# Performance work log

Measured on AMD Instinct MI355X. Metric: run time of the kernel, lower is better.

The kernel has to match this reference:

```python
import jax, jax.numpy as jnp
import numpy as np

D_MODEL = 1024
NUM_HEADS = 16
D_K = D_MODEL // NUM_HEADS
NEG_INF = -1e9


def setup_inputs() -> dict:
    key = jax.random.key(0)
    ks = jax.random.split(key, 9)
    B, S, D = 4, 2048, D_MODEL
    scale = 1.0 / np.sqrt(D)
    inp = {
        "x": jax.random.normal(ks[0], (B, S, D), dtype=jnp.float32),
        "Wq": jax.random.normal(ks[1], (D, D), dtype=jnp.float32) * scale,
        "bq": jnp.zeros((D,), dtype=jnp.float32),
        "Wk": jax.random.normal(ks[2], (D, D), dtype=jnp.float32) * scale,
        "bk": jnp.zeros((D,), dtype=jnp.float32),
        "Wv": jax.random.normal(ks[3], (D, D), dtype=jnp.float32) * scale,
        "bv": jnp.zeros((D,), dtype=jnp.float32),
        "Wo": jax.random.normal(ks[4], (D, D), dtype=jnp.float32) * scale,
        "bo": jnp.zeros((D,), dtype=jnp.float32),
    }
    return inp


def reference(x, Wq, bq, Wk, bk, Wv, bv, Wo, bo):
    B, S, D = x.shape
    H, dk = NUM_HEADS, D_K
    # padding mask: token is pad if any feature == 0; shape [B,1,1,S] (keys)
    mask = (x == 0).any(axis=-1)[:, None, None, :]

    def split_heads(t):  # [B,S,D] -> [B,H,S,dk]
        return t.reshape(B, S, H, dk).transpose(0, 2, 1, 3)

    q = split_heads(x @ Wq + bq)
    k = split_heads(x @ Wk + bk)
    v = split_heads(x @ Wv + bv)

    scores = jnp.einsum("bhqd,bhkd->bhqk", q, k) / np.sqrt(dk).astype(x.dtype)
    scores = jnp.where(mask, jnp.asarray(NEG_INF, x.dtype), scores)
    weights = jax.nn.softmax(scores, axis=-1)
    context = jnp.einsum("bhqk,bhkd->bhqd", weights, v)
    context = context.transpose(0, 2, 1, 3).reshape(B, S, D)
    return context @ Wo + bo
```

## Files before the change

kernel.cpp:

```cpp
#include <hip/hip_runtime.h>
#include <cstdint>
#include <cstddef>

static constexpr int Bz = 4, S = 2048, Dm = 1024, H = 16, DK = 64;
static constexpr int M = Bz * S;

typedef __attribute__((ext_vector_type(8))) short bf16x8;
typedef __attribute__((ext_vector_type(4))) float f32x4;

__device__ __forceinline__ unsigned short f2b(float f) {
    unsigned u = __float_as_uint(f);
    return (unsigned short)((u + 0x7FFFu + ((u >> 16) & 1u)) >> 16);
}

__device__ __forceinline__ unsigned cvtpk(float lo, float hi) {
    unsigned r;
    asm("v_cvt_pk_bf16_f32 %0, %1, %2" : "=v"(r) : "v"(lo), "v"(hi));
    return r;
}

__device__ __forceinline__ float fexp2(float x) {
#if __has_builtin(__builtin_amdgcn_exp2f)
    return __builtin_amdgcn_exp2f(x);
#else
    float r;
    asm("v_exp_f32 %0, %1" : "=v"(r) : "v"(x));
    return r;
#endif
}

__device__ __forceinline__ void gld_lds16(const void* g, void* l) {
    __builtin_amdgcn_global_load_lds(
        (const __attribute__((address_space(1))) unsigned int*)g,
        (__attribute__((address_space(3))) unsigned int*)l, 16, 0, 0);
}

__global__ __launch_bounds__(256) void k_convx(const float* __restrict__ x,
                                               unsigned short* __restrict__ xb,
                                               unsigned char* __restrict__ mask) {
    const int row = blockIdx.x;
    const int t = threadIdx.x;
    const float4 v = *(const float4*)(x + (size_t)row * Dm + t * 4);
    const bool z = (v.x == 0.f) | (v.y == 0.f) | (v.z == 0.f) | (v.w == 0.f);
    ushort4 o;
    o.x = f2b(v.x); o.y = f2b(v.y); o.z = f2b(v.z); o.w = f2b(v.w);
    *(ushort4*)(xb + (size_t)row * Dm + t * 4) = o;
    __shared__ int zf;
    if (t == 0) zf = 0;
    __syncthreads();
    if (z) zf = 1;
    __syncthreads();
    if (t == 0) mask[row] = (unsigned char)zf;
}

__global__ __launch_bounds__(256) void k_convw(const float* __restrict__ Wq, const float* __restrict__ Wk,
                                               const float* __restrict__ Wv, const float* __restrict__ Wo,
                                               unsigned short* __restrict__ Wt) {
    const float* W = (blockIdx.z == 0) ? Wq : (blockIdx.z == 1) ? Wk : (blockIdx.z == 2) ? Wv : Wo;
    unsigned short* o = Wt + (size_t)blockIdx.z * Dm * Dm;
    __shared__ float tile[32][33];
    const int k0 = blockIdx.x * 32, n0 = blockIdx.y * 32;
    const int tx = threadIdx.x, ty = threadIdx.y;
#pragma unroll
    for (int i = 0; i < 4; i++)
        tile[ty + 8 * i][tx] = W[(size_t)(k0 + ty + 8 * i) * Dm + n0 + tx];
    __syncthreads();
#pragma unroll
    for (int i = 0; i < 4; i++)
        o[(size_t)(n0 + ty + 8 * i) * Dm + k0 + tx] = f2b(tile[tx][ty + 8 * i]);
}

template <int MODE>
__global__ __launch_bounds__(256) void k_gemm(
    const unsigned short* __restrict__ A,
    const unsigned short* __restrict__ Bw,
    const float* __restrict__ bias0, const float* __restrict__ bias1, const float* __restrict__ bias2,
    unsigned short* __restrict__ Qo, unsigned short* __restrict__ Ko,
    unsigned short* __restrict__ Vto, float* __restrict__ Co)
{
    __shared__ unsigned short sA[128 * 32];
    __shared__ unsigned short sB[128 * 32];
    const int m0 = blockIdx.x * 128;
    const int gn0 = blockIdx.y * 128;
    const int tid = threadIdx.x;
    const int lane = tid & 63;
    const int wid = tid >> 6;
    const int wm = wid & 1, wn = wid >> 1;
    const int srow = tid >> 2;
    const int sc8 = (tid & 3) * 8;
    const int lr = lane & 15;
    const int lg = lane >> 4;
    f32x4 acc[4][4] = {};
    const unsigned short* Ag = A + (size_t)(m0 + srow) * Dm + sc8;
    const unsigned short* Bg = Bw + (size_t)(gn0 + srow) * Dm + sc8;
    unsigned short* const lA = sA + wid * 512;
    unsigned short* const lB = sB + wid * 512;
    for (int k0 = 0; k0 < Dm; k0 += 32) {
        __syncthreads();
        gld_lds16(Ag + k0, lA);
        gld_lds16(Ag + (size_t)64 * Dm + k0, lA + 2048);
        gld_lds16(Bg + k0, lB);
        gld_lds16(Bg + (size_t)64 * Dm + k0, lB + 2048);
        __syncthreads();
        bf16x8 af[4], bg[4];
#pragma unroll
        for (int mi = 0; mi < 4; mi++)
            af[mi] = *(const bf16x8*)&sA[(wm * 64 + mi * 16 + lr) * 32 + lg * 8];
#pragma unroll
        for (int ni = 0; ni < 4; ni++)
            bg[ni] = *(const bf16x8*)&sB[(wn * 64 + ni * 16 + lr) * 32 + lg * 8];
#pragma unroll
        for (int mi = 0; mi < 4; mi++)
#pragma unroll
            for (int ni = 0; ni < 4; ni++)
                acc[mi][ni] = __builtin_amdgcn_mfma_f32_16x16x32_bf16(af[mi], bg[ni], acc[mi][ni], 0, 0, 0);
    }
#pragma unroll
    for (int mi = 0; mi < 4; mi++) {
        const int row0 = m0 + wm * 64 + mi * 16 + lg * 4;
#pragma unroll
        for (int ni = 0; ni < 4; ni++) {
            const int gn = gn0 + wn * 64 + ni * 16 + lr;
            const int t = gn >> 10;
            const int n = gn & 1023;
            const int h = n >> 6, d = n & 63;
            const float bsv = (MODE == 0)
                ? ((t == 0) ? bias0[n] : (t == 1) ? bias1[n] : bias2[n])
                : bias0[gn];
#pragma unroll
            for (int r = 0; r < 4; r++) {
                const int row = row0 + r;
                const float v = acc[mi][ni][r] + bsv;
                if (MODE == 0) {
                    const int bb = row >> 11;
                    const int s = row & (S - 1);
                    const size_t bh = (size_t)bb * H + h;
                    if (t == 0) {
                        Qo[(bh * S + s) * DK + d] = f2b(v * 0.18033688011f);
                    } else if (t == 1) {
                        Ko[(bh * S + s) * DK + d] = f2b(v);
                    } else {
                        const int k5 = s & 31;
                        const int sp = (s & ~31) | ((k5 & 12) << 1) | ((k5 >> 4) << 2) | (k5 & 3);
                        Vto[(bh * DK + d) * S + sp] = f2b(v);
                    }
                } else {
                    Co[(size_t)row * Dm + gn] = v;
                }
            }
        }
    }
}

__global__ __launch_bounds__(512, 2) void k_attn(
    const unsigned short* __restrict__ Q, const unsigned short* __restrict__ K,
    const unsigned short* __restrict__ Vt, const unsigned char* __restrict__ mask,
    unsigned short* __restrict__ ctx)
{
    __shared__ unsigned short sK[2 * 4096];
    __shared__ unsigned short sV[2 * 4096];
    const int wg = blockIdx.x;
    const int sz = (wg & 7) * 64 + (wg >> 3);
    const int xt = sz & 7;
    const int bh = sz >> 3;
    const int bidx = bh >> 4, h = bh & 15;
    const int tid = threadIdx.x, lane = tid & 63, wid = tid >> 6;
    const int lr = lane & 15, lg = lane >> 4;
    const int qbase = xt * 256 + wid * 32;
    const size_t hoff = (size_t)bh * S * DK;
    const unsigned short* qp = Q + hoff + (size_t)(qbase + lr) * DK;
    const bf16x8 aqA0 = *(const bf16x8*)(qp + lg * 8);
    const bf16x8 aqA1 = *(const bf16x8*)(qp + 32 + lg * 8);
    const bf16x8 aqB0 = *(const bf16x8*)(qp + 16 * DK + lg * 8);
    const bf16x8 aqB1 = *(const bf16x8*)(qp + 16 * DK + 32 + lg * 8);
    const unsigned char* mrow = mask + bidx * S;
    f32x4 oA[4] = {}, oB[4] = {};
    f32x4 lvA = {}, lvB = {};
    const int rw = lane >> 3;
    const int row0 = wid * 8 + rw;
    const int csrc = ((lane & 7) ^ rw) << 4;
    const char* gK = (const char*)(K + hoff) + (size_t)row0 * 128 + csrc;
    const char* gV = (const char*)(Vt + hoff) + (size_t)row0 * (S * 2) + csrc;
    constexpr int NT = S / 64;
    unsigned short* const wK = sK + wid * 512;
    unsigned short* const wV = sV + wid * 512;

    gld_lds16(gK, wK);
    gld_lds16(gV, wV);
    unsigned char mb = mrow[lane];
    gK += 8192; gV += 128;

    auto body = [&](int t, const char* sKc, const char* sVc, int nbuf) {
        asm volatile("s_waitcnt vmcnt(0)" ::: "memory");
        __builtin_amdgcn_s_barrier();
        __builtin_amdgcn_sched_barrier(0);
        const unsigned char mbc = mb;
        if (t + 1 < NT) {
            gld_lds16(gK, wK + nbuf * 4096);
            gld_lds16(gV, wV + nbuf * 4096);
            mb = mrow[(t + 1) * 64 + lane];
            gK += 8192; gV += 128;
        }
        const unsigned long long bal = __ballot(mbc != 0);
        f32x4 zA[4], zB[4];
        __builtin_amdgcn_s_setprio(1);
#pragma unroll
        for (int nt = 0; nt < 4; nt++) {
            const int row = nt * 16 + lr;
            const int sw = (row & 7) << 4;
            const bf16x8 kf0 = *(const bf16x8*)(sKc + ((row * 128 + lg * 16) ^ sw));
            const bf16x8 kf1 = *(const bf16x8*)(sKc + ((row * 128 + 64 + lg * 16) ^ sw));
            f32x4 a = {};
            a = __builtin_amdgcn_mfma_f32_16x16x32_bf16(kf0, aqA0, a, 0, 0, 0);
            zA[nt] = __builtin_amdgcn_mfma_f32_16x16x32_bf16(kf1, aqA1, a, 0, 0, 0);
            f32x4 b = {};
            b = __builtin_amdgcn_mfma_f32_16x16x32_bf16(kf0, aqB0, b, 0, 0, 0);
            zB[nt] = __builtin_amdgcn_mfma_f32_16x16x32_bf16(kf1, aqB1, b, 0, 0, 0);
        }
        __builtin_amdgcn_s_setprio(0);
        if (bal) {
#pragma unroll
            for (int nt = 0; nt < 4; nt++)
#pragma unroll
                for (int r = 0; r < 4; r++)
                    if ((bal >> (nt * 16 + lg * 4 + r)) & 1) { zA[nt][r] = -1e9f; zB[nt][r] = -1e9f; }
        }
        union { unsigned u[4]; bf16x8 v; } wA0, wA1, wB0, wB1;
#pragma unroll
        for (int nt = 0; nt < 4; nt++) {
#pragma unroll
            for (int r = 0; r < 4; r++) zA[nt][r] = fexp2(zA[nt][r]);
            lvA += zA[nt];
        }
        wA0.u[0] = cvtpk(zA[0][0], zA[0][1]); wA0.u[1] = cvtpk(zA[0][2], zA[0][3]);
        wA0.u[2] = cvtpk(zA[1][0], zA[1][1]); wA0.u[3] = cvtpk(zA[1][2], zA[1][3]);
        wA1.u[0] = cvtpk(zA[2][0], zA[2][1]); wA1.u[1] = cvtpk(zA[2][2], zA[2][3]);
        wA1.u[2] = cvtpk(zA[3][0], zA[3][1]); wA1.u[3] = cvtpk(zA[3][2], zA[3][3]);
#pragma unroll
        for (int nt = 0; nt < 4; nt++) {
#pragma unroll
            for (int r = 0; r < 4; r++) zB[nt][r] = fexp2(zB[nt][r]);
            lvB += zB[nt];
        }
        wB0.u[0] = cvtpk(zB[0][0], zB[0][1]); wB0.u[1] = cvtpk(zB[0][2], zB[0][3]);
        wB0.u[2] = cvtpk(zB[1][0], zB[1][1]); wB0.u[3] = cvtpk(zB[1][2], zB[1][3]);
        wB1.u[0] = cvtpk(zB[2][0], zB[2][1]); wB1.u[1] = cvtpk(zB[2][2], zB[2][3]);
        wB1.u[2] = cvtpk(zB[3][0], zB[3][1]); wB1.u[3] = cvtpk(zB[3][2], zB[3][3]);
        __builtin_amdgcn_s_setprio(1);
#pragma unroll
        for (int dt = 0; dt < 4; dt++) {
            const int row = dt * 16 + lr;
            const int sw = (row & 7) << 4;
            const bf16x8 v0 = *(const bf16x8*)(sVc + ((row * 128 + lg * 16) ^ sw));
            const bf16x8 v1 = *(const bf16x8*)(sVc + ((row * 128 + 64 + lg * 16) ^ sw));
            oA[dt] = __builtin_amdgcn_mfma_f32_16x16x32_bf16(wA0.v, v0, oA[dt], 0, 0, 0);
            oA[dt] = __builtin_amdgcn_mfma_f32_16x16x32_bf16(wA1.v, v1, oA[dt], 0, 0, 0);
            oB[dt] = __builtin_amdgcn_mfma_f32_16x16x32_bf16(wB0.v, v0, oB[dt], 0, 0, 0);
            oB[dt] = __builtin_amdgcn_mfma_f32_16x16x32_bf16(wB1.v, v1, oB[dt], 0, 0, 0);
        }
        __builtin_amdgcn_s_setprio(0);
        asm volatile("s_waitcnt lgkmcnt(0)" ::: "memory");
    };

    const char* const sKb0 = (const char*)sK;
    const char* const sKb1 = sKb0 + 8192;
    const char* const sVb0 = (const char*)sV;
    const char* const sVb1 = sVb0 + 8192;
    for (int t = 0; t < NT; t += 2) {
        body(t,     sKb0, sVb0, 1);
        body(t + 1, sKb1, sVb1, 0);
    }

    float lsA = (lvA[0] + lvA[1]) + (lvA[2] + lvA[3]);
    lsA += __shfl_xor(lsA, 16, 64);
    lsA += __shfl_xor(lsA, 32, 64);
    float lsB = (lvB[0] + lvB[1]) + (lvB[2] + lvB[3]);
    lsB += __shfl_xor(lsB, 16, 64);
    lsB += __shfl_xor(lsB, 32, 64);
#pragma unroll
    for (int r = 0; r < 4; r++) {
        const float iA = 1.f / __shfl(lsA, lg * 4 + r, 16);
        const float iB = 1.f / __shfl(lsB, lg * 4 + r, 16);
        const int sA_ = qbase + lg * 4 + r;
#pragma unroll
        for (int dt = 0; dt < 4; dt++) {
            const int col = h * 64 + dt * 16 + lr;
            ctx[((size_t)bidx * S + sA_) * Dm + col]      = f2b(oA[dt][r] * iA);
            ctx[((size_t)bidx * S + sA_ + 16) * Dm + col] = f2b(oB[dt][r] * iB);
        }
    }
}

extern "C" void kernel_launch(void* const* d_in, const int* in_sizes, int n_in,
                              void* d_out, int out_size, void* d_ws, size_t ws_size,
                              hipStream_t stream)
{
    (void)in_sizes; (void)n_in; (void)out_size; (void)ws_size;
    const float* x  = (const float*)d_in[0];
    const float* Wq = (const float*)d_in[1];
    const float* bq = (const float*)d_in[2];
    const float* Wk = (const float*)d_in[3];
    const float* bk = (const float*)d_in[4];
    const float* Wv = (const float*)d_in[5];
    const float* bv = (const float*)d_in[6];
    const float* Wo = (const float*)d_in[7];
    const float* bo = (const float*)d_in[8];
    float* out = (float*)d_out;
    char* ws = (char*)d_ws;
    unsigned short* xb  = (unsigned short*)(ws);
    unsigned short* Wt  = (unsigned short*)(ws + ((size_t)16 << 20));
    unsigned short* Qb  = (unsigned short*)(ws + ((size_t)24 << 20));
    unsigned short* Kb  = (unsigned short*)(ws + ((size_t)40 << 20));
    unsigned short* Vtb = (unsigned short*)(ws + ((size_t)56 << 20));
    unsigned short* ctx = (unsigned short*)(ws + ((size_t)72 << 20));
    unsigned char*  msk = (unsigned char*)(ws + ((size_t)88 << 20));

    k_convx<<<dim3(M), dim3(256), 0, stream>>>(x, xb, msk);
    k_convw<<<dim3(Dm / 32, Dm / 32, 4), dim3(32, 8), 0, stream>>>(Wq, Wk, Wv, Wo, Wt);
    k_gemm<0><<<dim3(M / 128, 3072 / 128), dim3(256), 0, stream>>>(
        xb, Wt, bq, bk, bv, Qb, Kb, Vtb, nullptr);
    k_attn<<<dim3(Bz * H * (S / 256)), dim3(512), 0, stream>>>(Qb, Kb, Vtb, msk, ctx);
    k_gemm<1><<<dim3(M / 128, 1024 / 128), dim3(256), 0, stream>>>(
        ctx, Wt + (size_t)3 * Dm * Dm, bo, nullptr, nullptr, nullptr, nullptr, nullptr, out);
}
```

Baseline: 207.9 us.

## Triple-buffer K/V tiles in attention with partial vmcnt waits and mask precheck

Moves the attention kernel's K/V LDS staging from double to triple buffering. Each tile now waits with vmcnt(2) instead of draining all loads, so two tiles are in flight while the current one is computed. It also scans the key-padding mask once up front and skips the per-tile mask ballot when no key is padded. LDS use grows from 32KB to 48KB per block, which may lower occupancy at two blocks per CU, and the loop tail needs special handling.

```diff
diff --git a/kernel.cpp b/kernel.cpp
--- a/kernel.cpp
+++ b/kernel.cpp
@@ -152,13 +152,16 @@
     }
 }
 
+#define WAITV2 asm volatile("s_waitcnt vmcnt(2)" ::: "memory")
+#define WAITV0 asm volatile("s_waitcnt vmcnt(0)" ::: "memory")
+
 __global__ __launch_bounds__(512, 2) void k_attn(
     const unsigned short* __restrict__ Q, const unsigned short* __restrict__ K,
     const unsigned short* __restrict__ Vt, const unsigned char* __restrict__ mask,
     unsigned short* __restrict__ ctx)
 {
-    __shared__ unsigned short sK[2 * 4096];
-    __shared__ unsigned short sV[2 * 4096];
+    __shared__ unsigned short sK[3 * 4096];
+    __shared__ unsigned short sV[3 * 4096];
     const int wg = blockIdx.x;
     const int sz = (wg & 7) * 64 + (wg >> 3);
     const int xt = sz & 7;
@@ -168,12 +171,16 @@
     const int lr = lane & 15, lg = lane >> 4;
     const int qbase = xt * 256 + wid * 32;
     const size_t hoff = (size_t)bh * S * DK;
+    const unsigned char* mrow = mask + bidx * S;
+    const uint4 mza = *(const uint4*)(mrow + lane * 32);
+    const uint4 mzb = *(const uint4*)(mrow + lane * 32 + 16);
+    const bool anymask =
+        __ballot((mza.x | mza.y | mza.z | mza.w | mzb.x | mzb.y | mzb.z | mzb.w) != 0) != 0ull;
     const unsigned short* qp = Q + hoff + (size_t)(qbase + lr) * DK;
     const bf16x8 aqA0 = *(const bf16x8*)(qp + lg * 8);
     const bf16x8 aqA1 = *(const bf16x8*)(qp + 32 + lg * 8);
     const bf16x8 aqB0 = *(const bf16x8*)(qp + 16 * DK + lg * 8);
     const bf16x8 aqB1 = *(const bf16x8*)(qp + 16 * DK + 32 + lg * 8);
-    const unsigned char* mrow = mask + bidx * S;
     f32x4 oA[4] = {}, oB[4] = {};
     f32x4 lvA = {}, lvB = {};
     const int rw = lane >> 3;
@@ -182,26 +189,26 @@
     const char* gK = (const char*)(K + hoff) + (size_t)row0 * 128 + csrc;
     const char* gV = (const char*)(Vt + hoff) + (size_t)row0 * (S * 2) + csrc;
     constexpr int NT = S / 64;
-    unsigned short* const wK = sK + wid * 512;
-    unsigned short* const wV = sV + wid * 512;
-
-    gld_lds16(gK, wK);
-    gld_lds16(gV, wV);
-    unsigned char mb = mrow[lane];
+    unsigned short* const dK0 = sK + wid * 512;
+    unsigned short* const dV0 = sV + wid * 512;
+
+    gld_lds16(gK, dK0);            gld_lds16(gV, dV0);
     gK += 8192; gV += 128;
-
-    auto body = [&](int t, const char* sKc, const char* sVc, int nbuf) {
-        asm volatile("s_waitcnt vmcnt(0)" ::: "memory");
+    gld_lds16(gK, dK0 + 4096);     gld_lds16(gV, dV0 + 4096);
+    gK += 8192; gV += 128;
+
+    auto body = [&](int t, const char* sKc, const char* sVc,
+                    unsigned short* dKn, unsigned short* dVn) {
         __builtin_amdgcn_s_barrier();
         __builtin_amdgcn_sched_barrier(0);
-        const unsigned char mbc = mb;
-        if (t + 1 < NT) {
-            gld_lds16(gK, wK + nbuf * 4096);
-            gld_lds16(gV, wV + nbuf * 4096);
-            mb = mrow[(t + 1) * 64 + lane];
+        if (t + 2 < NT) {
+            gld_lds16(gK, dKn);
+            gld_lds16(gV, dVn);
             gK += 8192; gV += 128;
         }
-        const unsigned long long bal = __ballot(mbc != 0);
+        unsigned long long bal = 0;
+        if (anymask)
+            bal = __ballot(mrow[t * 64 + lane] != 0);
         f32x4 zA[4], zB[4];
         __builtin_amdgcn_s_setprio(1);
 #pragma unroll
@@ -262,14 +269,24 @@
         asm volatile("s_waitcnt lgkmcnt(0)" ::: "memory");
     };
 
-    const char* const sKb0 = (const char*)sK;
-    const char* const sKb1 = sKb0 + 8192;
-    const char* const sVb0 = (const char*)sV;
-    const char* const sVb1 = sVb0 + 8192;
-    for (int t = 0; t < NT; t += 2) {
-        body(t,     sKb0, sVb0, 1);
-        body(t + 1, sKb1, sVb1, 0);
+    const char* const bK0 = (const char*)sK;
+    const char* const bK1 = bK0 + 8192;
+    const char* const bK2 = bK0 + 16384;
+    const char* const bV0 = (const char*)sV;
+    const char* const bV1 = bV0 + 8192;
+    const char* const bV2 = bV0 + 16384;
+    unsigned short* const dK1 = dK0 + 4096;
+    unsigned short* const dV1 = dV0 + 4096;
+    unsigned short* const dK2 = dK0 + 8192;
+    unsigned short* const dV2 = dV0 + 8192;
+
+    for (int t = 0; t < NT - 2; t += 3) {
+        WAITV2; body(t,     bK0, bV0, dK2, dV2);
+        WAITV2; body(t + 1, bK1, bV1, dK0, dV0);
+        WAITV2; body(t + 2, bK2, bV2, dK1, dV1);
     }
+    WAITV2; body(NT - 2, bK0, bV0, dK2, dV2);
+    WAITV0; body(NT - 1, bK1, bV1, dK2, dV2);
 
     float lsA = (lvA[0] + lvA[1]) + (lvA[2] + lvA[3]);
     lsA += __shfl_xor(lsA, 16, 64);
```

New measurement: 208.3 us. About the same (+0.1%).

## Add double-buffered, swizzled 256x128 QKV projection GEMM kernel

Applied to the files above, without the earlier changes.

Replaces the generic QKV projection GEMM with a dedicated kernel. It uses 256x128 tiles with 512 threads, a K-step of 64, double-buffered LDS filled by direct global-to-LDS loads, an XOR-swizzled layout to avoid bank conflicts, and MFMA phases raised in priority so they overlap the next stage's prefetch. The aim is to cut memory stalls and LDS conflicts in the largest GEMM. In exchange it uses more LDS per block (96 KB), which limits occupancy to one block per CU. The output GEMM is simplified to a plain bias-add epilogue.

```diff
diff --git a/kernel.cpp b/kernel.cpp
--- a/kernel.cpp
+++ b/kernel.cpp
@@ -70,13 +70,124 @@
         o[(size_t)(n0 + ty + 8 * i) * Dm + k0 + tx] = f2b(tile[tx][ty + 8 * i]);
 }
 
+__global__ __launch_bounds__(512, 1) void k_g0(
+    const unsigned short* __restrict__ A,
+    const unsigned short* __restrict__ Bw,
+    const float* __restrict__ bq, const float* __restrict__ bk, const float* __restrict__ bv,
+    unsigned short* __restrict__ Qo, unsigned short* __restrict__ Ko,
+    unsigned short* __restrict__ Vto)
+{
+    __shared__ unsigned short sA[2][256 * 64];
+    __shared__ unsigned short sB[2][128 * 64];
+    const int m0 = blockIdx.x * 256;
+    const int n0 = blockIdx.y * 128;
+    const int tid = threadIdx.x;
+    const int lane = tid & 63;
+    const int wid = tid >> 6;
+    const int wm = wid >> 1;
+    const int wn = wid & 1;
+    const int lr = lane & 15, lg = lane >> 4;
+    f32x4 acc[4][4] = {};
+
+    const int csrc = ((lane & 7) ^ (lane >> 3)) << 4;
+    const char* gA = (const char*)A + (size_t)(m0 + (tid >> 3)) * (Dm * 2) + csrc;
+    const char* gB = (const char*)Bw + (size_t)(n0 + (tid >> 3)) * (Dm * 2) + csrc;
+
+    auto stage = [&](int buf, int ktn) {
+        const char* a = gA + ktn * 128;
+        const char* b = gB + ktn * 128;
+#pragma unroll
+        for (int j = 0; j < 4; j++)
+            gld_lds16(a + (size_t)j * 64 * (Dm * 2), &sA[buf][0] + j * 4096 + wid * 512);
+#pragma unroll
+        for (int j = 0; j < 2; j++)
+            gld_lds16(b + (size_t)j * 64 * (Dm * 2), &sB[buf][0] + j * 4096 + wid * 512);
+    };
+
+    auto phase = [&](const char* rA, const char* rB, int q, bool dostage, int nbuf, int ktn) {
+        bf16x8 af[2][2], bfr[4][2];
+#pragma unroll
+        for (int m2 = 0; m2 < 2; m2++) {
+            const int row = wm * 64 + (q * 2 + m2) * 16 + lr;
+            const int sw = row & 7;
+            af[m2][0] = *(const bf16x8*)(rA + row * 128 + ((lg ^ sw) << 4));
+            af[m2][1] = *(const bf16x8*)(rA + row * 128 + (((4 + lg) ^ sw) << 4));
+        }
+#pragma unroll
+        for (int ni = 0; ni < 4; ni++) {
+            const int row = wn * 64 + ni * 16 + lr;
+            const int sw = row & 7;
+            bfr[ni][0] = *(const bf16x8*)(rB + row * 128 + ((lg ^ sw) << 4));
+            bfr[ni][1] = *(const bf16x8*)(rB + row * 128 + (((4 + lg) ^ sw) << 4));
+        }
+        if (dostage) stage(nbuf, ktn);
+        __builtin_amdgcn_s_barrier();
+        asm volatile("s_waitcnt lgkmcnt(0)" ::: "memory");
+        __builtin_amdgcn_sched_barrier(0);
+        __builtin_amdgcn_s_setprio(1);
+#pragma unroll
+        for (int m2 = 0; m2 < 2; m2++)
+#pragma unroll
+            for (int ni = 0; ni < 4; ni++) {
+                acc[q * 2 + m2][ni] = __builtin_amdgcn_mfma_f32_16x16x32_bf16(
+                    af[m2][0], bfr[ni][0], acc[q * 2 + m2][ni], 0, 0, 0);
+                acc[q * 2 + m2][ni] = __builtin_amdgcn_mfma_f32_16x16x32_bf16(
+                    af[m2][1], bfr[ni][1], acc[q * 2 + m2][ni], 0, 0, 0);
+            }
+        __builtin_amdgcn_s_setprio(0);
+        __builtin_amdgcn_s_barrier();
+    };
+
+    stage(0, 0);
+    int cur = 0;
+    for (int kt = 0; kt < Dm / 64; kt++) {
+        asm volatile("s_waitcnt vmcnt(0)" ::: "memory");
+        __builtin_amdgcn_s_barrier();
+        const char* rA = (const char*)&sA[cur][0];
+        const char* rB = (const char*)&sB[cur][0];
+        const bool st = (kt + 1 < Dm / 64);
+        phase(rA, rB, 0, st, cur ^ 1, kt + 1);
+        phase(rA, rB, 1, false, 0, 0);
+        cur ^= 1;
+    }
+
+#pragma unroll
+    for (int mi = 0; mi < 4; mi++) {
+        const int row0 = m0 + wm * 64 + mi * 16 + lg * 4;
+#pragma unroll
+        for (int ni = 0; ni < 4; ni++) {
+            const int gn = n0 + wn * 64 + ni * 16 + lr;
+            const int t = gn >> 10;
+            const int n = gn & 1023;
+            const int h = n >> 6, d = n & 63;
+            const float bsv = (t == 0) ? bq[n] : (t == 1) ? bk[n] : bv[n];
+#pragma unroll
+            for (int r = 0; r < 4; r++) {
+                const int row = row0 + r;
+                const float v = acc[mi][ni][r] + bsv;
+                const int bb = row >> 11;
+                const int s = row & (S - 1);
+                const size_t bh = (size_t)bb * H + h;
+                if (t == 0) {
+                    Qo[(bh * S + s) * DK + d] = f2b(v * 0.18033688011f);
+                } else if (t == 1) {
+                    Ko[(bh * S + s) * DK + d] = f2b(v);
+                } else {
+                    const int k5 = s & 31;
+                    const int sp = (s & ~31) | ((k5 & 12) << 1) | ((k5 >> 4) << 2) | (k5 & 3);
+                    Vto[(bh * DK + d) * S + sp] = f2b(v);
+                }
+            }
+        }
+    }
+}
+
 template <int MODE>
 __global__ __launch_bounds__(256) void k_gemm(
     const unsigned short* __restrict__ A,
     const unsigned short* __restrict__ Bw,
-    const float* __restrict__ bias0, const float* __restrict__ bias1, const float* __restrict__ bias2,
-    unsigned short* __restrict__ Qo, unsigned short* __restrict__ Ko,
-    unsigned short* __restrict__ Vto, float* __restrict__ Co)
+    const float* __restrict__ bias0,
+    float* __restrict__ Co)
 {
     __shared__ unsigned short sA[128 * 32];
     __shared__ unsigned short sB[128 * 32];
@@ -121,33 +232,10 @@
 #pragma unroll
         for (int ni = 0; ni < 4; ni++) {
             const int gn = gn0 + wn * 64 + ni * 16 + lr;
-            const int t = gn >> 10;
-            const int n = gn & 1023;
-            const int h = n >> 6, d = n & 63;
-            const float bsv = (MODE == 0)
-                ? ((t == 0) ? bias0[n] : (t == 1) ? bias1[n] : bias2[n])
-                : bias0[gn];
-#pragma unroll
-            for (int r = 0; r < 4; r++) {
-                const int row = row0 + r;
-                const float v = acc[mi][ni][r] + bsv;
-                if (MODE == 0) {
-                    const int bb = row >> 11;
-                    const int s = row & (S - 1);
-                    const size_t bh = (size_t)bb * H + h;
-                    if (t == 0) {
-                        Qo[(bh * S + s) * DK + d] = f2b(v * 0.18033688011f);
-                    } else if (t == 1) {
-                        Ko[(bh * S + s) * DK + d] = f2b(v);
-                    } else {
-                        const int k5 = s & 31;
-                        const int sp = (s & ~31) | ((k5 & 12) << 1) | ((k5 >> 4) << 2) | (k5 & 3);
-                        Vto[(bh * DK + d) * S + sp] = f2b(v);
-                    }
-                } else {
-                    Co[(size_t)row * Dm + gn] = v;
-                }
-            }
+            const float bsv = bias0[gn];
+#pragma unroll
+            for (int r = 0; r < 4; r++)
+                Co[(size_t)(row0 + r) * Dm + gn] = acc[mi][ni][r] + bsv;
         }
     }
 }
@@ -317,9 +405,9 @@
 
     k_convx<<<dim3(M), dim3(256), 0, stream>>>(x, xb, msk);
     k_convw<<<dim3(Dm / 32, Dm / 32, 4), dim3(32, 8), 0, stream>>>(Wq, Wk, Wv, Wo, Wt);
-    k_gemm<0><<<dim3(M / 128, 3072 / 128), dim3(256), 0, stream>>>(
-        xb, Wt, bq, bk, bv, Qb, Kb, Vtb, nullptr);
+    k_g0<<<dim3(M / 256, 3072 / 128), dim3(512), 0, stream>>>(
+        xb, Wt, bq, bk, bv, Qb, Kb, Vtb);
     k_attn<<<dim3(Bz * H * (S / 256)), dim3(512), 0, stream>>>(Qb, Kb, Vtb, msk, ctx);
     k_gemm<1><<<dim3(M / 128, 1024 / 128), dim3(256), 0, stream>>>(
-        ctx, Wt + (size_t)3 * Dm * Dm, bo, nullptr, nullptr, nullptr, nullptr, nullptr, out);
-}
+        ctx, Wt + (size_t)3 * Dm * Dm, bo, out);
+}
```

After: 216.6 us. 4.2% more time.
